# Optimization experiments

Measured on AMD Instinct MI355X. Metric: run time of the kernel, lower is better.

Reference implementation:

```python
import jax, jax.numpy as jnp
import numpy as np

ALPHA = 0.1  # LeakyReLU negative slope
F_OUT = 128

def _leaky(x):
    return jnp.where(x >= 0, x, ALPHA * x)

def setup_inputs() -> dict:
    key = jax.random.key(0)
    ks = jax.random.split(key, 12)
    B, N, F_IN = 4, 4096, 128
    q = jax.random.normal(ks[0], (B, N, F_IN), jnp.float32)
    k = jax.random.normal(ks[1], (B, N, F_IN), jnp.float32)
    v = jax.random.normal(ks[2], (B, N, F_IN), jnp.float32)
    adj = jax.random.randint(ks[3], (B, N, N), 0, 2, jnp.int32)
    s = 1.0 / np.sqrt(F_IN)
    Wq_w = jax.random.uniform(ks[4], (F_OUT, F_IN), jnp.float32, -s, s)
    Wq_b = jax.random.uniform(ks[5], (F_OUT,), jnp.float32, -s, s)
    Wk_w = jax.random.uniform(ks[6], (F_OUT, F_IN), jnp.float32, -s, s)
    Wk_b = jax.random.uniform(ks[7], (F_OUT,), jnp.float32, -s, s)
    Wv_w = jax.random.uniform(ks[8], (F_OUT, F_IN), jnp.float32, -s, s)
    Wv_b = jax.random.uniform(ks[9], (F_OUT,), jnp.float32, -s, s)
    # xavier_uniform with gain=1.414 on (2F,1)
    lim = 1.414 * np.sqrt(6.0 / (2 * F_OUT + 1))
    a = jax.random.uniform(ks[10], (2 * F_OUT, 1), jnp.float32, -lim, lim)
    so = 1.0 / np.sqrt(F_OUT)
    Wo_w = jax.random.uniform(ks[11], (F_OUT, F_OUT), jnp.float32, -so, so)
    return {"q": q, "k": k, "v": v, "adj": adj, "Wq_w": Wq_w, "Wq_b": Wq_b,
            "Wk_w": Wk_w, "Wk_b": Wk_b, "Wv_w": Wv_w, "Wv_b": Wv_b,
            "a": a, "Wo_w": Wo_w}

def reference(q, k, v, adj, Wq_w, Wq_b, Wk_w, Wk_b, Wv_w, Wv_b, a, Wo_w):
    qp = q @ Wq_w.T + Wq_b                      # (B,N,F)
    kp = k @ Wk_w.T + Wk_b
    vp = v @ Wv_w.T + Wv_b
    Wh1 = qp @ a[:F_OUT]                        # (B,N,1)
    Wh2 = kp @ a[F_OUT:]                        # (B,N,1)
    e = _leaky(Wh1 + jnp.swapaxes(Wh2, 1, 2))   # (B,N,N)
    e = jnp.where(adj > 0, e, jnp.float32(-1e9))
    att = jax.nn.softmax(e, axis=-1)
    h = jnp.einsum('bnm,bmf->bnf', att, vp)     # (B,N,F)
    return _leaky(h @ Wo_w.T)
```

## Files before the change

### kernel.cpp

```cpp
#include <hip/hip_runtime.h>


constexpr int B = 4, N = 4096, F = 128;
constexpr int BN = B * N;
constexpr int BK = 64;
constexpr int SPLITS = 4;
constexpr int JC = N / SPLITS;
constexpr int NIT = JC / BK;
#define ALPHA 0.1f

using float4v = __attribute__((ext_vector_type(4))) float;
using short8 = __attribute__((ext_vector_type(8))) short;

__device__ __forceinline__ float leaky(float x) { return x >= 0.f ? x : ALPHA * x; }
__device__ __forceinline__ unsigned short f2bf(float x) {
    unsigned u = __float_as_uint(x);
    u = (u + 0x7FFFu + ((u >> 16) & 1u)) >> 16;
    return (unsigned short)u;
}
__device__ __forceinline__ unsigned pack_bf2(float lo, float hi) {
    unsigned a = __float_as_uint(lo), b2 = __float_as_uint(hi);
    a = a + 0x7FFFu + ((a >> 16) & 1u);
    b2 = b2 + 0x7FFFu + ((b2 >> 16) & 1u);
    return __builtin_amdgcn_perm(b2, a, 0x07060302u);
}

__global__ void k_prep(const float* __restrict__ Wq_w, const float* __restrict__ Wq_b,
                       const float* __restrict__ Wk_w, const float* __restrict__ Wk_b,
                       const float* __restrict__ a, float* __restrict__ c1,
                       float* __restrict__ c2, float* __restrict__ d12) {
    __shared__ float as[2 * F];
    __shared__ float red[2 * F];
    int t = threadIdx.x;
    as[t] = a[t];
    __syncthreads();
    int f = t & 127;
    const float* W = (t < F) ? Wq_w : Wk_w;
    const float* ao = (t < F) ? as : as + F;
    float s = 0.f;
#pragma unroll 8
    for (int o = 0; o < F; o++) s = fmaf(W[o * F + f], ao[o], s);
    if (t < F) c1[f] = s; else c2[f] = s;
    red[t] = (t < F) ? Wq_b[f] * as[f] : Wk_b[f] * as[F + f];
    __syncthreads();
    for (int st = 64; st > 0; st >>= 1) {
        if (f < st) red[t] += red[t + st];
        __syncthreads();
    }
    if (t == 0) d12[0] = red[0];
    if (t == F) d12[1] = red[F];
}

__global__ void k_wh(const float* __restrict__ q, const float* __restrict__ k,
                     const float* __restrict__ c1, const float* __restrict__ c2,
                     const float* __restrict__ d12,
                     float* __restrict__ Wh1, float* __restrict__ Wh2) {
    __shared__ float c1s[F], c2s[F];
    int t = threadIdx.x;
    if (t < F) c1s[t] = c1[t]; else c2s[t - F] = c2[t - F];
    __syncthreads();
    int row = blockIdx.x * 8 + (t >> 5);
    int lane = t & 31;
    float4 q4 = reinterpret_cast<const float4*>(q)[row * 32 + lane];
    float4 k4 = reinterpret_cast<const float4*>(k)[row * 32 + lane];
    float s1 = q4.x * c1s[lane * 4 + 0] + q4.y * c1s[lane * 4 + 1] +
               q4.z * c1s[lane * 4 + 2] + q4.w * c1s[lane * 4 + 3];
    float s2 = k4.x * c2s[lane * 4 + 0] + k4.y * c2s[lane * 4 + 1] +
               k4.z * c2s[lane * 4 + 2] + k4.w * c2s[lane * 4 + 3];
    for (int m = 16; m > 0; m >>= 1) { s1 += __shfl_xor(s1, m); s2 += __shfl_xor(s2, m); }
    if (lane == 0) { Wh1[row] = s1 + d12[0]; Wh2[row] = s2 + d12[1]; }
}

__global__ void k_max2(const float* __restrict__ Wh2, float* __restrict__ M2) {
    int b = blockIdx.x, t = threadIdx.x;
    float m = -1e30f;
    for (int i = t; i < N; i += 256) m = fmaxf(m, Wh2[b * N + i]);
    __shared__ float red[256];
    red[t] = m;
    __syncthreads();
    for (int s = 128; s > 0; s >>= 1) { if (t < s) red[t] = fmaxf(red[t], red[t + s]); __syncthreads(); }
    if (t == 0) M2[b] = red[0];
}

__global__ void k_tab(const float* __restrict__ Wh1, const float* __restrict__ Wh2,
                      const float* __restrict__ M2,
                      float* __restrict__ P1, float* __restrict__ Q1,
                      float* __restrict__ P2, float* __restrict__ Q2) {
    int i = blockIdx.x * 256 + threadIdx.x;
    int b = i >> 12;
    float w1 = Wh1[i], w2 = Wh2[i];
    float mi = leaky(w1 + M2[b]);
    P1[i] = __expf(w1 - mi);
    Q1[i] = __expf(ALPHA * w1 - mi);
    P2[i] = __expf(w2);
    Q2[i] = __expf(ALPHA * w2);
}

__global__ __launch_bounds__(256) void k_vp(const float* __restrict__ v,
                                            const float* __restrict__ Wv_w,
                                            const float* __restrict__ Wv_b,
                                            unsigned short* __restrict__ vpT) {
    __shared__ float vs[32][F];
    __shared__ float Ws[F][129];
    __shared__ unsigned short ts[F][40];
    int t = threadIdx.x;
    int row0g = blockIdx.x * 32;
    int b = row0g >> 12;
    int row0 = row0g & (N - 1);
    {
        const float4* src = reinterpret_cast<const float4*>(v + row0g * F);
        float4* dst = reinterpret_cast<float4*>(&vs[0][0]);
#pragma unroll
        for (int u = 0; u < 4; u++) dst[u * 256 + t] = src[u * 256 + t];
    }
    {
        const float4* src = reinterpret_cast<const float4*>(Wv_w);
#pragma unroll
        for (int u = 0; u < 16; u++) {
            int unit = u * 256 + t;
            int r = unit >> 5, s = unit & 31;
            float4 val = src[unit];
            Ws[r][s * 4 + 0] = val.x; Ws[r][s * 4 + 1] = val.y;
            Ws[r][s * 4 + 2] = val.z; Ws[r][s * 4 + 3] = val.w;
        }
    }
    int f = t & 127, g = t >> 7;
    float bias = Wv_b[f];
    __syncthreads();
    float acc[16];
#pragma unroll
    for (int r = 0; r < 16; r++) acc[r] = bias;
    for (int kk = 0; kk < F; kk++) {
        float wk = Ws[f][kk];
#pragma unroll
        for (int r = 0; r < 16; r++) acc[r] = fmaf(vs[g * 16 + r][kk], wk, acc[r]);
    }
#pragma unroll
    for (int r = 0; r < 16; r++) ts[f][g * 16 + r] = f2bf(acc[r]);
    __syncthreads();
    int fr = t >> 1, hseg = t & 1;
    uint4 d0 = *reinterpret_cast<uint4*>(&ts[fr][hseg * 16]);
    uint4 d1 = *reinterpret_cast<uint4*>(&ts[fr][hseg * 16 + 8]);
    unsigned short* dst = vpT + ((size_t)(b * F + fr) * N + row0 + hseg * 16);
    *reinterpret_cast<uint4*>(dst) = d0;
    *reinterpret_cast<uint4*>(dst + 8) = d1;
}

__global__ __launch_bounds__(256, 2) void k_attn(
    const unsigned short* __restrict__ vpT, const int* __restrict__ adj,
    const float* __restrict__ Wh1, const float* __restrict__ P1, const float* __restrict__ Q1,
    const float* __restrict__ P2, const float* __restrict__ Q2, const float* __restrict__ Wh2,
    float* __restrict__ h_part, float* __restrict__ den_part) {
    __shared__ __align__(16) unsigned short bs[2][F][72];
    __shared__ __align__(16) float sP2[JC], sQ2[JC], sW2[JC];
    int t = threadIdx.x;
    int idx = blockIdx.x;
    int split = idx & 3;
    int tile = (idx >> 2) & 31;
    int b = idx >> 7;
    int i0 = tile * 128;
    int jb0 = split * JC;
    int widx = t >> 6, lane = t & 63, m = lane & 15, q = lane >> 4;
    int r0 = i0 + widx * 32;

    {
        reinterpret_cast<float4*>(sP2)[t] = reinterpret_cast<const float4*>(P2 + b * N + jb0)[t];
        reinterpret_cast<float4*>(sQ2)[t] = reinterpret_cast<const float4*>(Q2 + b * N + jb0)[t];
        reinterpret_cast<float4*>(sW2)[t] = reinterpret_cast<const float4*>(Wh2 + b * N + jb0)[t];
    }

    int gi0 = b * N + r0 + m;
    int gi1 = gi0 + 16;
    float p1a = P1[gi0], q1a = Q1[gi0], t1a = -Wh1[gi0];
    float p1b = P1[gi1], q1b = Q1[gi1], t1b = -Wh1[gi1];

    const unsigned short* vb = vpT + (size_t)b * F * N + jb0;
    const int* adjbase = adj + (size_t)gi0 * N + jb0 + q * 8;

    uint4 sreg[4];
    int4 aregA[8], aregB[8];

    auto load_stage = [&](int it) {
#pragma unroll
        for (int u = 0; u < 4; u++) {
            int unit = u * 256 + t;
            int r = unit >> 3, s = unit & 7;
            sreg[u] = *reinterpret_cast<const uint4*>(vb + (size_t)r * N + it * BK + s * 8);
        }
    };
    auto write_stage = [&](int pb) {
#pragma unroll
        for (int u = 0; u < 4; u++) {
            int unit = u * 256 + t;
            int r = unit >> 3, s = unit & 7;
            *reinterpret_cast<uint4*>(&bs[pb][r][s * 8]) = sreg[u];
        }
    };
    auto load_adj = [&](int it, int4* ar) {
#pragma unroll
        for (int rt = 0; rt < 2; rt++)
#pragma unroll
            for (int kh = 0; kh < 2; kh++) {
                const int* p = adjbase + (size_t)rt * 16 * N + it * BK + kh * 32;
                ar[(rt * 2 + kh) * 2 + 0] = *reinterpret_cast<const int4*>(p);
                ar[(rt * 2 + kh) * 2 + 1] = *reinterpret_cast<const int4*>(p + 4);
            }
    };

    float4v acc0[8], acc1[8];
#pragma unroll
    for (int nt = 0; nt < 8; nt++) {
        acc0[nt] = (float4v){0.f, 0.f, 0.f, 0.f};
        acc1[nt] = (float4v){0.f, 0.f, 0.f, 0.f};
    }
    float den0 = 0.f, den1 = 0.f;

    auto gen_af = [&](const int4& a0, const int4& a1, const float4& x2a, const float4& x2b,
                      const float4& p2a, const float4& p2b, const float4& q2a, const float4& q2b,
                      float p1, float q1, float t1, float& den) -> short8 {
        float w0 = a0.x ? ((x2a.x >= t1) ? p1 * p2a.x : q1 * q2a.x) : 0.f;
        float w1 = a0.y ? ((x2a.y >= t1) ? p1 * p2a.y : q1 * q2a.y) : 0.f;
        float w2 = a0.z ? ((x2a.z >= t1) ? p1 * p2a.z : q1 * q2a.z) : 0.f;
        float w3 = a0.w ? ((x2a.w >= t1) ? p1 * p2a.w : q1 * q2a.w) : 0.f;
        float w4 = a1.x ? ((x2b.x >= t1) ? p1 * p2b.x : q1 * q2b.x) : 0.f;
        float w5 = a1.y ? ((x2b.y >= t1) ? p1 * p2b.y : q1 * q2b.y) : 0.f;
        float w6 = a1.z ? ((x2b.z >= t1) ? p1 * p2b.z : q1 * q2b.z) : 0.f;
        float w7 = a1.w ? ((x2b.w >= t1) ? p1 * p2b.w : q1 * q2b.w) : 0.f;
        den += ((w0 + w1) + (w2 + w3)) + ((w4 + w5) + (w6 + w7));
        union { short8 s; uint4 u; } r;
        r.u.x = pack_bf2(w0, w1); r.u.y = pack_bf2(w2, w3);
        r.u.z = pack_bf2(w4, w5); r.u.w = pack_bf2(w6, w7);
        return r.s;
    };

    auto body = [&](int it, int4* cur, int4* nxt, int pb) {
        if (it + 1 < NIT) {
            load_stage(it + 1);
            load_adj(it + 1, nxt);
        }
#pragma unroll
        for (int kh = 0; kh < 2; kh++) {
            int jl = it * BK + kh * 32 + q * 8;
            float4 x2a = *reinterpret_cast<const float4*>(&sW2[jl]);
            float4 x2b = *reinterpret_cast<const float4*>(&sW2[jl + 4]);
            float4 p2a = *reinterpret_cast<const float4*>(&sP2[jl]);
            float4 p2b = *reinterpret_cast<const float4*>(&sP2[jl + 4]);
            float4 q2a = *reinterpret_cast<const float4*>(&sQ2[jl]);
            float4 q2b = *reinterpret_cast<const float4*>(&sQ2[jl + 4]);
            short8 af0 = gen_af(cur[kh * 2 + 0], cur[kh * 2 + 1], x2a, x2b, p2a, p2b, q2a, q2b,
                                p1a, q1a, t1a, den0);
            short8 af1 = gen_af(cur[(2 + kh) * 2 + 0], cur[(2 + kh) * 2 + 1], x2a, x2b, p2a, p2b,
                                q2a, q2b, p1b, q1b, t1b, den1);
#pragma unroll
            for (int nt = 0; nt < 8; nt++) {
                short8 bf = *reinterpret_cast<const short8*>(&bs[pb][nt * 16 + m][kh * 32 + q * 8]);
                acc0[nt] = __builtin_amdgcn_mfma_f32_16x16x32_bf16(af0, bf, acc0[nt], 0, 0, 0);
                acc1[nt] = __builtin_amdgcn_mfma_f32_16x16x32_bf16(af1, bf, acc1[nt], 0, 0, 0);
            }
        }
        if (it + 1 < NIT) write_stage(pb ^ 1);
        __syncthreads();
    };

    load_stage(0);
    load_adj(0, aregA);
    write_stage(0);
    __syncthreads();

#pragma unroll 1
    for (int ith = 0; ith < NIT / 2; ith++) {
        body(ith * 2 + 0, aregA, aregB, 0);
        body(ith * 2 + 1, aregB, aregA, 1);
    }

    den0 += __shfl_xor(den0, 16); den0 += __shfl_xor(den0, 32);
    den1 += __shfl_xor(den1, 16); den1 += __shfl_xor(den1, 32);
    float* dp = den_part + (size_t)split * BN;
    if (q == 0) { dp[gi0] = den0; dp[gi1] = den1; }
    float* hp = h_part + (size_t)split * BN * F;
    int orow0 = b * N + r0 + q * 4;
#pragma unroll
    for (int nt = 0; nt < 8; nt++)
#pragma unroll
        for (int r = 0; r < 4; r++) {
            hp[(size_t)(orow0 + r) * F + nt * 16 + m] = acc0[nt][r];
            hp[(size_t)(orow0 + 16 + r) * F + nt * 16 + m] = acc1[nt][r];
        }
}

__global__ __launch_bounds__(256) void k_out(const float* __restrict__ h_part,
                                             const float* __restrict__ den_part,
                                             const float* __restrict__ Wo_w,
                                             float* __restrict__ out) {
    __shared__ float hs[32][F];
    __shared__ float Ws[F][129];
    int t = threadIdx.x;
    int row0 = blockIdx.x * 32;
    {
        const float4* src = reinterpret_cast<const float4*>(Wo_w);
#pragma unroll
        for (int u = 0; u < 16; u++) {
            int unit = u * 256 + t;
            int r = unit >> 5, s = unit & 31;
            float4 val = src[unit];
            Ws[r][s * 4 + 0] = val.x; Ws[r][s * 4 + 1] = val.y;
            Ws[r][s * 4 + 2] = val.z; Ws[r][s * 4 + 3] = val.w;
        }
    }
#pragma unroll
    for (int u = 0; u < 4; u++) {
        int unit = u * 256 + t;
        int r = unit >> 5, s = unit & 31;
        size_t off = (size_t)(row0 + r) * F + s * 4;
        float4 h0 = *reinterpret_cast<const float4*>(h_part + off);
        float4 h1 = *reinterpret_cast<const float4*>(h_part + (size_t)BN * F + off);
        float4 h2 = *reinterpret_cast<const float4*>(h_part + (size_t)2 * BN * F + off);
        float4 h3 = *reinterpret_cast<const float4*>(h_part + (size_t)3 * BN * F + off);
        float dsum = den_part[row0 + r] + den_part[BN + row0 + r] +
                     den_part[2 * BN + row0 + r] + den_part[3 * BN + row0 + r];
        float inv = 1.f / dsum;
        hs[r][s * 4 + 0] = (h0.x + h1.x + h2.x + h3.x) * inv;
        hs[r][s * 4 + 1] = (h0.y + h1.y + h2.y + h3.y) * inv;
        hs[r][s * 4 + 2] = (h0.z + h1.z + h2.z + h3.z) * inv;
        hs[r][s * 4 + 3] = (h0.w + h1.w + h2.w + h3.w) * inv;
    }
    __syncthreads();
    int f = t & 127, g = t >> 7;
    float acc[16];
#pragma unroll
    for (int r = 0; r < 16; r++) acc[r] = 0.f;
    for (int kk = 0; kk < F; kk++) {
        float wk = Ws[f][kk];
#pragma unroll
        for (int r = 0; r < 16; r++) acc[r] = fmaf(hs[g * 16 + r][kk], wk, acc[r]);
    }
#pragma unroll
    for (int r = 0; r < 16; r++) out[(size_t)(row0 + g * 16 + r) * F + f] = leaky(acc[r]);
}

extern "C" void kernel_launch(void* const* d_in, const int* in_sizes, int n_in,
                              void* d_out, int out_size, void* d_ws, size_t ws_size,
                              hipStream_t stream) {
    const float* q    = (const float*)d_in[0];
    const float* k    = (const float*)d_in[1];
    const float* v    = (const float*)d_in[2];
    const int*   adj  = (const int*)d_in[3];
    const float* Wq_w = (const float*)d_in[4];
    const float* Wq_b = (const float*)d_in[5];
    const float* Wk_w = (const float*)d_in[6];
    const float* Wk_b = (const float*)d_in[7];
    const float* Wv_w = (const float*)d_in[8];
    const float* Wv_b = (const float*)d_in[9];
    const float* a    = (const float*)d_in[10];
    const float* Wo_w = (const float*)d_in[11];
    float* out = (float*)d_out;
    float* ws = (float*)d_ws;

    unsigned short* vpT = (unsigned short*)ws;
    float* h_part   = ws + BN * F / 2;
    float* den_part = h_part + (size_t)SPLITS * BN * F;
    float* Wh1 = den_part + SPLITS * BN;
    float* Wh2 = Wh1 + BN;
    float* P1  = Wh2 + BN;
    float* Q1  = P1 + BN;
    float* P2  = Q1 + BN;
    float* Q2  = P2 + BN;
    float* c1  = Q2 + BN;
    float* c2  = c1 + F;
    float* d12 = c2 + F;
    float* M2  = d12 + 2;

    k_prep<<<1, 256, 0, stream>>>(Wq_w, Wq_b, Wk_w, Wk_b, a, c1, c2, d12);
    k_wh<<<BN / 8, 256, 0, stream>>>(q, k, c1, c2, d12, Wh1, Wh2);
    k_max2<<<B, 256, 0, stream>>>(Wh2, M2);
    k_tab<<<BN / 256, 256, 0, stream>>>(Wh1, Wh2, M2, P1, Q1, P2, Q2);
    k_vp<<<BN / 32, 256, 0, stream>>>(v, Wv_w, Wv_b, vpT);
    k_attn<<<B * 32 * SPLITS, 256, 0, stream>>>(vpT, adj, Wh1, P1, Q1, P2, Q2, Wh2,
                                                h_part, den_part);
    k_out<<<BN / 32, 256, 0, stream>>>(h_part, den_part, Wo_w, out);
}
```

Baseline: 508.7 us.

## Drop split-K in attention and fuse output projection into attention kernel

```diff
diff --git a/kernel.cpp b/kernel.cpp
--- a/kernel.cpp
+++ b/kernel.cpp
@@ -4,9 +4,7 @@
 constexpr int B = 4, N = 4096, F = 128;
 constexpr int BN = B * N;
 constexpr int BK = 64;
-constexpr int SPLITS = 4;
-constexpr int JC = N / SPLITS;
-constexpr int NIT = JC / BK;
+constexpr int NIT = N / BK;
 #define ALPHA 0.1f
 
 using float4v = __attribute__((ext_vector_type(4))) float;
@@ -146,39 +144,53 @@
     *reinterpret_cast<uint4*>(dst + 8) = d1;
 }
 
-__global__ __launch_bounds__(256, 2) void k_attn(
+constexpr int LDS_BS_BYTES = 2 * F * 72 * 2;
+constexpr int LDS_LOOP_BYTES = LDS_BS_BYTES + 3 * N * 4;
+constexpr int LDS_TAIL_BYTES = 64 * 129 * 4 + F * 129 * 4;
+constexpr int LDS_BYTES = LDS_TAIL_BYTES;
+
+__global__ __launch_bounds__(256, 1) void k_attn(
     const unsigned short* __restrict__ vpT, const int* __restrict__ adj,
     const float* __restrict__ Wh1, const float* __restrict__ P1, const float* __restrict__ Q1,
     const float* __restrict__ P2, const float* __restrict__ Q2, const float* __restrict__ Wh2,
-    float* __restrict__ h_part, float* __restrict__ den_part) {
-    __shared__ __align__(16) unsigned short bs[2][F][72];
-    __shared__ __align__(16) float sP2[JC], sQ2[JC], sW2[JC];
+    const float* __restrict__ Wo_w, float* __restrict__ out) {
+    __shared__ __align__(16) char smem[LDS_BYTES];
+    auto bs = reinterpret_cast<unsigned short(*)[F][72]>(smem);
+    float* sP2 = reinterpret_cast<float*>(smem + LDS_BS_BYTES);
+    float* sQ2 = sP2 + N;
+    float* sW2 = sQ2 + N;
+
     int t = threadIdx.x;
     int idx = blockIdx.x;
-    int split = idx & 3;
-    int tile = (idx >> 2) & 31;
-    int b = idx >> 7;
-    int i0 = tile * 128;
-    int jb0 = split * JC;
+    int tile = idx & 63;
+    int b = idx >> 6;
+    int i0 = tile * 64;
     int widx = t >> 6, lane = t & 63, m = lane & 15, q = lane >> 4;
-    int r0 = i0 + widx * 32;
+    int r0 = i0 + widx * 16;
 
     {
-        reinterpret_cast<float4*>(sP2)[t] = reinterpret_cast<const float4*>(P2 + b * N + jb0)[t];
-        reinterpret_cast<float4*>(sQ2)[t] = reinterpret_cast<const float4*>(Q2 + b * N + jb0)[t];
-        reinterpret_cast<float4*>(sW2)[t] = reinterpret_cast<const float4*>(Wh2 + b * N + jb0)[t];
+        const float4* gp = reinterpret_cast<const float4*>(P2 + (size_t)b * N);
+        const float4* gq = reinterpret_cast<const float4*>(Q2 + (size_t)b * N);
+        const float4* gw = reinterpret_cast<const float4*>(Wh2 + (size_t)b * N);
+        float4* dp = reinterpret_cast<float4*>(sP2);
+        float4* dq = reinterpret_cast<float4*>(sQ2);
+        float4* dw = reinterpret_cast<float4*>(sW2);
+#pragma unroll
+        for (int u = 0; u < 4; u++) {
+            dp[u * 256 + t] = gp[u * 256 + t];
+            dq[u * 256 + t] = gq[u * 256 + t];
+            dw[u * 256 + t] = gw[u * 256 + t];
+        }
     }
 
     int gi0 = b * N + r0 + m;
-    int gi1 = gi0 + 16;
     float p1a = P1[gi0], q1a = Q1[gi0], t1a = -Wh1[gi0];
-    float p1b = P1[gi1], q1b = Q1[gi1], t1b = -Wh1[gi1];
-
-    const unsigned short* vb = vpT + (size_t)b * F * N + jb0;
-    const int* adjbase = adj + (size_t)gi0 * N + jb0 + q * 8;
+
+    const unsigned short* vb = vpT + (size_t)b * F * N;
+    const int* adjbase = adj + (size_t)gi0 * N + q * 8;
 
     uint4 sreg[4];
-    int4 aregA[8], aregB[8];
+    int4 aregA[4], aregB[4];
 
     auto load_stage = [&](int it) {
 #pragma unroll
@@ -198,22 +210,17 @@
     };
     auto load_adj = [&](int it, int4* ar) {
 #pragma unroll
-        for (int rt = 0; rt < 2; rt++)
-#pragma unroll
-            for (int kh = 0; kh < 2; kh++) {
-                const int* p = adjbase + (size_t)rt * 16 * N + it * BK + kh * 32;
-                ar[(rt * 2 + kh) * 2 + 0] = *reinterpret_cast<const int4*>(p);
-                ar[(rt * 2 + kh) * 2 + 1] = *reinterpret_cast<const int4*>(p + 4);
-            }
-    };
-
-    float4v acc0[8], acc1[8];
-#pragma unroll
-    for (int nt = 0; nt < 8; nt++) {
-        acc0[nt] = (float4v){0.f, 0.f, 0.f, 0.f};
-        acc1[nt] = (float4v){0.f, 0.f, 0.f, 0.f};
-    }
-    float den0 = 0.f, den1 = 0.f;
+        for (int kh = 0; kh < 2; kh++) {
+            const int* p = adjbase + it * BK + kh * 32;
+            ar[kh * 2 + 0] = *reinterpret_cast<const int4*>(p);
+            ar[kh * 2 + 1] = *reinterpret_cast<const int4*>(p + 4);
+        }
+    };
+
+    float4v acc0[8];
+#pragma unroll
+    for (int nt = 0; nt < 8; nt++) acc0[nt] = (float4v){0.f, 0.f, 0.f, 0.f};
+    float den0 = 0.f;
 
     auto gen_af = [&](const int4& a0, const int4& a1, const float4& x2a, const float4& x2b,
                       const float4& p2a, const float4& p2b, const float4& q2a, const float4& q2b,
@@ -249,13 +256,10 @@
             float4 q2b = *reinterpret_cast<const float4*>(&sQ2[jl + 4]);
             short8 af0 = gen_af(cur[kh * 2 + 0], cur[kh * 2 + 1], x2a, x2b, p2a, p2b, q2a, q2b,
                                 p1a, q1a, t1a, den0);
-            short8 af1 = gen_af(cur[(2 + kh) * 2 + 0], cur[(2 + kh) * 2 + 1], x2a, x2b, p2a, p2b,
-                                q2a, q2b, p1b, q1b, t1b, den1);
 #pragma unroll
             for (int nt = 0; nt < 8; nt++) {
                 short8 bf = *reinterpret_cast<const short8*>(&bs[pb][nt * 16 + m][kh * 32 + q * 8]);
                 acc0[nt] = __builtin_amdgcn_mfma_f32_16x16x32_bf16(af0, bf, acc0[nt], 0, 0, 0);
-                acc1[nt] = __builtin_amdgcn_mfma_f32_16x16x32_bf16(af1, bf, acc1[nt], 0, 0, 0);
             }
         }
         if (it + 1 < NIT) write_stage(pb ^ 1);
@@ -273,29 +277,12 @@
         body(ith * 2 + 1, aregB, aregA, 1);
     }
 
-    den0 += __shfl_xor(den0, 16); den0 += __shfl_xor(den0, 32);
-    den1 += __shfl_xor(den1, 16); den1 += __shfl_xor(den1, 32);
-    float* dp = den_part + (size_t)split * BN;
-    if (q == 0) { dp[gi0] = den0; dp[gi1] = den1; }
-    float* hp = h_part + (size_t)split * BN * F;
-    int orow0 = b * N + r0 + q * 4;
-#pragma unroll
-    for (int nt = 0; nt < 8; nt++)
-#pragma unroll
-        for (int r = 0; r < 4; r++) {
-            hp[(size_t)(orow0 + r) * F + nt * 16 + m] = acc0[nt][r];
-            hp[(size_t)(orow0 + 16 + r) * F + nt * 16 + m] = acc1[nt][r];
-        }
-}
-
-__global__ __launch_bounds__(256) void k_out(const float* __restrict__ h_part,
-                                             const float* __restrict__ den_part,
-                                             const float* __restrict__ Wo_w,
-                                             float* __restrict__ out) {
-    __shared__ float hs[32][F];
-    __shared__ float Ws[F][129];
-    int t = threadIdx.x;
-    int row0 = blockIdx.x * 32;
+    den0 += __shfl_xor(den0, 16);
+    den0 += __shfl_xor(den0, 32);
+
+    float (*hs)[129] = reinterpret_cast<float(*)[129]>(smem);
+    float (*Ws)[129] = reinterpret_cast<float(*)[129]>(smem + 64 * 129 * 4);
+
     {
         const float4* src = reinterpret_cast<const float4*>(Wo_w);
 #pragma unroll
@@ -308,34 +295,26 @@
         }
     }
 #pragma unroll
-    for (int u = 0; u < 4; u++) {
-        int unit = u * 256 + t;
-        int r = unit >> 5, s = unit & 31;
-        size_t off = (size_t)(row0 + r) * F + s * 4;
-        float4 h0 = *reinterpret_cast<const float4*>(h_part + off);
-        float4 h1 = *reinterpret_cast<const float4*>(h_part + (size_t)BN * F + off);
-        float4 h2 = *reinterpret_cast<const float4*>(h_part + (size_t)2 * BN * F + off);
-        float4 h3 = *reinterpret_cast<const float4*>(h_part + (size_t)3 * BN * F + off);
-        float dsum = den_part[row0 + r] + den_part[BN + row0 + r] +
-                     den_part[2 * BN + row0 + r] + den_part[3 * BN + row0 + r];
-        float inv = 1.f / dsum;
-        hs[r][s * 4 + 0] = (h0.x + h1.x + h2.x + h3.x) * inv;
-        hs[r][s * 4 + 1] = (h0.y + h1.y + h2.y + h3.y) * inv;
-        hs[r][s * 4 + 2] = (h0.z + h1.z + h2.z + h3.z) * inv;
-        hs[r][s * 4 + 3] = (h0.w + h1.w + h2.w + h3.w) * inv;
-    }
-    __syncthreads();
+    for (int r = 0; r < 4; r++) {
+        float inv = 1.f / __shfl(den0, q * 4 + r);
+#pragma unroll
+        for (int nt = 0; nt < 8; nt++)
+            hs[widx * 16 + q * 4 + r][nt * 16 + m] = acc0[nt][r] * inv;
+    }
+    __syncthreads();
+
     int f = t & 127, g = t >> 7;
-    float acc[16];
-#pragma unroll
-    for (int r = 0; r < 16; r++) acc[r] = 0.f;
+    float acc[32];
+#pragma unroll
+    for (int r = 0; r < 32; r++) acc[r] = 0.f;
     for (int kk = 0; kk < F; kk++) {
         float wk = Ws[f][kk];
 #pragma unroll
-        for (int r = 0; r < 16; r++) acc[r] = fmaf(hs[g * 16 + r][kk], wk, acc[r]);
-    }
-#pragma unroll
-    for (int r = 0; r < 16; r++) out[(size_t)(row0 + g * 16 + r) * F + f] = leaky(acc[r]);
+        for (int r = 0; r < 32; r++) acc[r] = fmaf(hs[g * 32 + r][kk], wk, acc[r]);
+    }
+    size_t obase = (size_t)(b * N + i0 + g * 32) * F + f;
+#pragma unroll
+    for (int r = 0; r < 32; r++) out[obase + (size_t)r * F] = leaky(acc[r]);
 }
 
 extern "C" void kernel_launch(void* const* d_in, const int* in_sizes, int n_in,
@@ -357,9 +336,7 @@
     float* ws = (float*)d_ws;
 
     unsigned short* vpT = (unsigned short*)ws;
-    float* h_part   = ws + BN * F / 2;
-    float* den_part = h_part + (size_t)SPLITS * BN * F;
-    float* Wh1 = den_part + SPLITS * BN;
+    float* Wh1 = ws + BN * F / 2;
     float* Wh2 = Wh1 + BN;
     float* P1  = Wh2 + BN;
     float* Q1  = P1 + BN;
@@ -375,7 +352,5 @@
     k_max2<<<B, 256, 0, stream>>>(Wh2, M2);
     k_tab<<<BN / 256, 256, 0, stream>>>(Wh1, Wh2, M2, P1, Q1, P2, Q2);
     k_vp<<<BN / 32, 256, 0, stream>>>(v, Wv_w, Wv_b, vpT);
-    k_attn<<<B * 32 * SPLITS, 256, 0, stream>>>(vpT, adj, Wh1, P1, Q1, P2, Q2, Wh2,
-                                                h_part, den_part);
-    k_out<<<BN / 32, 256, 0, stream>>>(h_part, den_part, Wo_w, out);
-}
+    k_attn<<<B * 64, 256, 0, stream>>>(vpT, adj, Wh1, P1, Q1, P2, Q2, Wh2, Wo_w, out);
+}
```

New measurement: 543.4 us. 1.07x slower.

## Drop LDS staging in attention kernel and split K across wave pairs

Applied to the files above, without the earlier changes.

```diff
diff --git a/kernel.cpp b/kernel.cpp
--- a/kernel.cpp
+++ b/kernel.cpp
@@ -4,9 +4,7 @@
 constexpr int B = 4, N = 4096, F = 128;
 constexpr int BN = B * N;
 constexpr int BK = 64;
-constexpr int SPLITS = 4;
-constexpr int JC = N / SPLITS;
-constexpr int NIT = JC / BK;
+constexpr int NIT = N / BK;
 #define ALPHA 0.1f
 
 using float4v = __attribute__((ext_vector_type(4))) float;
@@ -151,141 +149,111 @@
     const float* __restrict__ Wh1, const float* __restrict__ P1, const float* __restrict__ Q1,
     const float* __restrict__ P2, const float* __restrict__ Q2, const float* __restrict__ Wh2,
     float* __restrict__ h_part, float* __restrict__ den_part) {
-    __shared__ __align__(16) unsigned short bs[2][F][72];
-    __shared__ __align__(16) float sP2[JC], sQ2[JC], sW2[JC];
     int t = threadIdx.x;
     int idx = blockIdx.x;
-    int split = idx & 3;
-    int tile = (idx >> 2) & 31;
+    int tile = idx & 127;
     int b = idx >> 7;
-    int i0 = tile * 128;
-    int jb0 = split * JC;
+    int i0 = tile * 32;
     int widx = t >> 6, lane = t & 63, m = lane & 15, q = lane >> 4;
-    int r0 = i0 + widx * 32;
-
+    int rt = widx >> 1;
+    int kh = widx & 1;
+    int r0 = i0 + rt * 16;
+
+    int gi0 = b * N + r0 + m;
+    float p1a = P1[gi0], q1a = Q1[gi0], t1a = -Wh1[gi0];
+
+    int jo = kh * 32 + q * 8;
+    const unsigned short* bfb = vpT + ((size_t)(b * F + m)) * N + jo;
+    const int* adjb = adj + (size_t)gi0 * N + jo;
+    const float* W2b = Wh2 + (size_t)b * N + jo;
+    const float* P2b = P2 + (size_t)b * N + jo;
+    const float* Q2b = Q2 + (size_t)b * N + jo;
+
+    float4v acc0[8];
+#pragma unroll
+    for (int nt = 0; nt < 8; nt++) acc0[nt] = (float4v){0.f, 0.f, 0.f, 0.f};
+    float den0 = 0.f;
+
+    auto body = [&](int it, const int4& a0, const int4& a1) {
+        const float* w = W2b + it * BK;
+        float4 x2a = *reinterpret_cast<const float4*>(w);
+        float4 x2b = *reinterpret_cast<const float4*>(w + 4);
+        const float* p = P2b + it * BK;
+        float4 p2a = *reinterpret_cast<const float4*>(p);
+        float4 p2b = *reinterpret_cast<const float4*>(p + 4);
+        const float* qq = Q2b + it * BK;
+        float4 q2a = *reinterpret_cast<const float4*>(qq);
+        float4 q2b = *reinterpret_cast<const float4*>(qq + 4);
+        const unsigned short* vr = bfb + it * BK;
+        short8 bf0 = *reinterpret_cast<const short8*>(vr);
+        short8 bf1 = *reinterpret_cast<const short8*>(vr + (size_t)1 * 16 * N);
+        short8 bf2 = *reinterpret_cast<const short8*>(vr + (size_t)2 * 16 * N);
+        short8 bf3 = *reinterpret_cast<const short8*>(vr + (size_t)3 * 16 * N);
+        short8 bf4 = *reinterpret_cast<const short8*>(vr + (size_t)4 * 16 * N);
+        short8 bf5 = *reinterpret_cast<const short8*>(vr + (size_t)5 * 16 * N);
+        short8 bf6 = *reinterpret_cast<const short8*>(vr + (size_t)6 * 16 * N);
+        short8 bf7 = *reinterpret_cast<const short8*>(vr + (size_t)7 * 16 * N);
+
+        float w0 = a0.x ? ((x2a.x >= t1a) ? p1a * p2a.x : q1a * q2a.x) : 0.f;
+        float w1 = a0.y ? ((x2a.y >= t1a) ? p1a * p2a.y : q1a * q2a.y) : 0.f;
+        float w2 = a0.z ? ((x2a.z >= t1a) ? p1a * p2a.z : q1a * q2a.z) : 0.f;
+        float w3 = a0.w ? ((x2a.w >= t1a) ? p1a * p2a.w : q1a * q2a.w) : 0.f;
+        float w4 = a1.x ? ((x2b.x >= t1a) ? p1a * p2b.x : q1a * q2b.x) : 0.f;
+        float w5 = a1.y ? ((x2b.y >= t1a) ? p1a * p2b.y : q1a * q2b.y) : 0.f;
+        float w6 = a1.z ? ((x2b.z >= t1a) ? p1a * p2b.z : q1a * q2b.z) : 0.f;
+        float w7 = a1.w ? ((x2b.w >= t1a) ? p1a * p2b.w : q1a * q2b.w) : 0.f;
+        den0 += ((w0 + w1) + (w2 + w3)) + ((w4 + w5) + (w6 + w7));
+        union { short8 s; uint4 u; } af;
+        af.u.x = pack_bf2(w0, w1); af.u.y = pack_bf2(w2, w3);
+        af.u.z = pack_bf2(w4, w5); af.u.w = pack_bf2(w6, w7);
+
+        acc0[0] = __builtin_amdgcn_mfma_f32_16x16x32_bf16(af.s, bf0, acc0[0], 0, 0, 0);
+        acc0[1] = __builtin_amdgcn_mfma_f32_16x16x32_bf16(af.s, bf1, acc0[1], 0, 0, 0);
+        acc0[2] = __builtin_amdgcn_mfma_f32_16x16x32_bf16(af.s, bf2, acc0[2], 0, 0, 0);
+        acc0[3] = __builtin_amdgcn_mfma_f32_16x16x32_bf16(af.s, bf3, acc0[3], 0, 0, 0);
+        acc0[4] = __builtin_amdgcn_mfma_f32_16x16x32_bf16(af.s, bf4, acc0[4], 0, 0, 0);
+        acc0[5] = __builtin_amdgcn_mfma_f32_16x16x32_bf16(af.s, bf5, acc0[5], 0, 0, 0);
+        acc0[6] = __builtin_amdgcn_mfma_f32_16x16x32_bf16(af.s, bf6, acc0[6], 0, 0, 0);
+        acc0[7] = __builtin_amdgcn_mfma_f32_16x16x32_bf16(af.s, bf7, acc0[7], 0, 0, 0);
+    };
+
+    int4 aA0, aA1, aB0, aB1;
     {
-        reinterpret_cast<float4*>(sP2)[t] = reinterpret_cast<const float4*>(P2 + b * N + jb0)[t];
-        reinterpret_cast<float4*>(sQ2)[t] = reinterpret_cast<const float4*>(Q2 + b * N + jb0)[t];
-        reinterpret_cast<float4*>(sW2)[t] = reinterpret_cast<const float4*>(Wh2 + b * N + jb0)[t];
-    }
-
-    int gi0 = b * N + r0 + m;
-    int gi1 = gi0 + 16;
-    float p1a = P1[gi0], q1a = Q1[gi0], t1a = -Wh1[gi0];
-    float p1b = P1[gi1], q1b = Q1[gi1], t1b = -Wh1[gi1];
-
-    const unsigned short* vb = vpT + (size_t)b * F * N + jb0;
-    const int* adjbase = adj + (size_t)gi0 * N + jb0 + q * 8;
-
-    uint4 sreg[4];
-    int4 aregA[8], aregB[8];
-
-    auto load_stage = [&](int it) {
-#pragma unroll
-        for (int u = 0; u < 4; u++) {
-            int unit = u * 256 + t;
-            int r = unit >> 3, s = unit & 7;
-            sreg[u] = *reinterpret_cast<const uint4*>(vb + (size_t)r * N + it * BK + s * 8);
-        }
-    };
-    auto write_stage = [&](int pb) {
-#pragma unroll
-        for (int u = 0; u < 4; u++) {
-            int unit = u * 256 + t;
-            int r = unit >> 3, s = unit & 7;
-            *reinterpret_cast<uint4*>(&bs[pb][r][s * 8]) = sreg[u];
-        }
-    };
-    auto load_adj = [&](int it, int4* ar) {
-#pragma unroll
-        for (int rt = 0; rt < 2; rt++)
-#pragma unroll
-            for (int kh = 0; kh < 2; kh++) {
-                const int* p = adjbase + (size_t)rt * 16 * N + it * BK + kh * 32;
-                ar[(rt * 2 + kh) * 2 + 0] = *reinterpret_cast<const int4*>(p);
-                ar[(rt * 2 + kh) * 2 + 1] = *reinterpret_cast<const int4*>(p + 4);
-            }
-    };
-
-    float4v acc0[8], acc1[8];
-#pragma unroll
-    for (int nt = 0; nt < 8; nt++) {
-        acc0[nt] = (float4v){0.f, 0.f, 0.f, 0.f};
-        acc1[nt] = (float4v){0.f, 0.f, 0.f, 0.f};
-    }
-    float den0 = 0.f, den1 = 0.f;
-
-    auto gen_af = [&](const int4& a0, const int4& a1, const float4& x2a, const float4& x2b,
-                      const float4& p2a, const float4& p2b, const float4& q2a, const float4& q2b,
-                      float p1, float q1, float t1, float& den) -> short8 {
-        float w0 = a0.x ? ((x2a.x >= t1) ? p1 * p2a.x : q1 * q2a.x) : 0.f;
-        float w1 = a0.y ? ((x2a.y >= t1) ? p1 * p2a.y : q1 * q2a.y) : 0.f;
-        float w2 = a0.z ? ((x2a.z >= t1) ? p1 * p2a.z : q1 * q2a.z) : 0.f;
-        float w3 = a0.w ? ((x2a.w >= t1) ? p1 * p2a.w : q1 * q2a.w) : 0.f;
-        float w4 = a1.x ? ((x2b.x >= t1) ? p1 * p2b.x : q1 * q2b.x) : 0.f;
-        float w5 = a1.y ? ((x2b.y >= t1) ? p1 * p2b.y : q1 * q2b.y) : 0.f;
-        float w6 = a1.z ? ((x2b.z >= t1) ? p1 * p2b.z : q1 * q2b.z) : 0.f;
-        float w7 = a1.w ? ((x2b.w >= t1) ? p1 * p2b.w : q1 * q2b.w) : 0.f;
-        den += ((w0 + w1) + (w2 + w3)) + ((w4 + w5) + (w6 + w7));
-        union { short8 s; uint4 u; } r;
-        r.u.x = pack_bf2(w0, w1); r.u.y = pack_bf2(w2, w3);
-        r.u.z = pack_bf2(w4, w5); r.u.w = pack_bf2(w6, w7);
-        return r.s;
-    };
-
-    auto body = [&](int it, int4* cur, int4* nxt, int pb) {
-        if (it + 1 < NIT) {
-            load_stage(it + 1);
-            load_adj(it + 1, nxt);
-        }
-#pragma unroll
-        for (int kh = 0; kh < 2; kh++) {
-            int jl = it * BK + kh * 32 + q * 8;
-            float4 x2a = *reinterpret_cast<const float4*>(&sW2[jl]);
-            float4 x2b = *reinterpret_cast<const float4*>(&sW2[jl + 4]);
-            float4 p2a = *reinterpret_cast<const float4*>(&sP2[jl]);
-            float4 p2b = *reinterpret_cast<const float4*>(&sP2[jl + 4]);
-            float4 q2a = *reinterpret_cast<const float4*>(&sQ2[jl]);
-            float4 q2b = *reinterpret_cast<const float4*>(&sQ2[jl + 4]);
-            short8 af0 = gen_af(cur[kh * 2 + 0], cur[kh * 2 + 1], x2a, x2b, p2a, p2b, q2a, q2b,
-                                p1a, q1a, t1a, den0);
-            short8 af1 = gen_af(cur[(2 + kh) * 2 + 0], cur[(2 + kh) * 2 + 1], x2a, x2b, p2a, p2b,
-                                q2a, q2b, p1b, q1b, t1b, den1);
-#pragma unroll
-            for (int nt = 0; nt < 8; nt++) {
-                short8 bf = *reinterpret_cast<const short8*>(&bs[pb][nt * 16 + m][kh * 32 + q * 8]);
-                acc0[nt] = __builtin_amdgcn_mfma_f32_16x16x32_bf16(af0, bf, acc0[nt], 0, 0, 0);
-                acc1[nt] = __builtin_amdgcn_mfma_f32_16x16x32_bf16(af1, bf, acc1[nt], 0, 0, 0);
-            }
-        }
-        if (it + 1 < NIT) write_stage(pb ^ 1);
-        __syncthreads();
-    };
-
-    load_stage(0);
-    load_adj(0, aregA);
-    write_stage(0);
-    __syncthreads();
-
+        const int* p0 = adjb;
+        aA0 = *reinterpret_cast<const int4*>(p0);
+        aA1 = *reinterpret_cast<const int4*>(p0 + 4);
+        const int* p1 = adjb + BK;
+        aB0 = *reinterpret_cast<const int4*>(p1);
+        aB1 = *reinterpret_cast<const int4*>(p1 + 4);
+    }
 #pragma unroll 1
     for (int ith = 0; ith < NIT / 2; ith++) {
-        body(ith * 2 + 0, aregA, aregB, 0);
-        body(ith * 2 + 1, aregB, aregA, 1);
-    }
-
-    den0 += __shfl_xor(den0, 16); den0 += __shfl_xor(den0, 32);
-    den1 += __shfl_xor(den1, 16); den1 += __shfl_xor(den1, 32);
-    float* dp = den_part + (size_t)split * BN;
-    if (q == 0) { dp[gi0] = den0; dp[gi1] = den1; }
-    float* hp = h_part + (size_t)split * BN * F;
-    int orow0 = b * N + r0 + q * 4;
+        int it = ith * 2;
+        body(it, aA0, aA1);
+        if (it + 2 < NIT) {
+            const int* p = adjb + (size_t)(it + 2) * BK;
+            aA0 = *reinterpret_cast<const int4*>(p);
+            aA1 = *reinterpret_cast<const int4*>(p + 4);
+        }
+        body(it + 1, aB0, aB1);
+        if (it + 3 < NIT) {
+            const int* p = adjb + (size_t)(it + 3) * BK;
+            aB0 = *reinterpret_cast<const int4*>(p);
+            aB1 = *reinterpret_cast<const int4*>(p + 4);
+        }
+    }
+
+    den0 += __shfl_xor(den0, 16);
+    den0 += __shfl_xor(den0, 32);
+    float* dp = den_part + (size_t)kh * BN;
+    if (lane < 16) dp[gi0] = den0;
+    float* hp = h_part + (size_t)kh * BN * F;
+    int orow0 = b * N + i0 + rt * 16 + q * 4;
 #pragma unroll
     for (int nt = 0; nt < 8; nt++)
 #pragma unroll
-        for (int r = 0; r < 4; r++) {
+        for (int r = 0; r < 4; r++)
             hp[(size_t)(orow0 + r) * F + nt * 16 + m] = acc0[nt][r];
-            hp[(size_t)(orow0 + 16 + r) * F + nt * 16 + m] = acc1[nt][r];
-        }
 }
 
 __global__ __launch_bounds__(256) void k_out(const float* __restrict__ h_part,
@@ -314,15 +282,12 @@
         size_t off = (size_t)(row0 + r) * F + s * 4;
         float4 h0 = *reinterpret_cast<const float4*>(h_part + off);
         float4 h1 = *reinterpret_cast<const float4*>(h_part + (size_t)BN * F + off);
-        float4 h2 = *reinterpret_cast<const float4*>(h_part + (size_t)2 * BN * F + off);
-        float4 h3 = *reinterpret_cast<const float4*>(h_part + (size_t)3 * BN * F + off);
-        float dsum = den_part[row0 + r] + den_part[BN + row0 + r] +
-                     den_part[2 * BN + row0 + r] + den_part[3 * BN + row0 + r];
+        float dsum = den_part[row0 + r] + den_part[BN + row0 + r];
         float inv = 1.f / dsum;
-        hs[r][s * 4 + 0] = (h0.x + h1.x + h2.x + h3.x) * inv;
-        hs[r][s * 4 + 1] = (h0.y + h1.y + h2.y + h3.y) * inv;
-        hs[r][s * 4 + 2] = (h0.z + h1.z + h2.z + h3.z) * inv;
-        hs[r][s * 4 + 3] = (h0.w + h1.w + h2.w + h3.w) * inv;
+        hs[r][s * 4 + 0] = (h0.x + h1.x) * inv;
+        hs[r][s * 4 + 1] = (h0.y + h1.y) * inv;
+        hs[r][s * 4 + 2] = (h0.z + h1.z) * inv;
+        hs[r][s * 4 + 3] = (h0.w + h1.w) * inv;
     }
     __syncthreads();
     int f = t & 127, g = t >> 7;
@@ -358,8 +323,8 @@
 
     unsigned short* vpT = (unsigned short*)ws;
     float* h_part   = ws + BN * F / 2;
-    float* den_part = h_part + (size_t)SPLITS * BN * F;
-    float* Wh1 = den_part + SPLITS * BN;
+    float* den_part = h_part + (size_t)2 * BN * F;
+    float* Wh1 = den_part + 2 * BN;
     float* Wh2 = Wh1 + BN;
     float* P1  = Wh2 + BN;
     float* Q1  = P1 + BN;
@@ -375,7 +340,7 @@
     k_max2<<<B, 256, 0, stream>>>(Wh2, M2);
     k_tab<<<BN / 256, 256, 0, stream>>>(Wh1, Wh2, M2, P1, Q1, P2, Q2);
     k_vp<<<BN / 32, 256, 0, stream>>>(v, Wv_w, Wv_b, vpT);
-    k_attn<<<B * 32 * SPLITS, 256, 0, stream>>>(vpT, adj, Wh1, P1, Q1, P2, Q2, Wh2,
-                                                h_part, den_part);
+    k_attn<<<B * 128, 256, 0, stream>>>(vpT, adj, Wh1, P1, Q1, P2, Q2, Wh2,
+                                        h_part, den_part);
     k_out<<<BN / 32, 256, 0, stream>>>(h_part, den_part, Wo_w, out);
 }
```

Result: slower. 583.7 us (+14.8%).
